# Kernel optimization log

Measured on AMD Instinct MI355X. Metric: run time of the kernel, lower is better.

The kernel has to match this reference:

```python
import jax, jax.numpy as jnp
import numpy as np

MARGIN_SCALE = 0.2
SPATIAL_ALPHA = 0.6
CHANNEL_ALPHA = 0.5
LANG_ALPHA = 0.4
EPS = 1e-06


def _xywh_to_xyxy(boxes):
    xc, yc, w, h = jnp.split(boxes, 4, axis=-1)
    return jnp.concatenate([xc - w / 2.0, yc - h / 2.0, xc + w / 2.0, yc + h / 2.0], axis=-1)


def _clamp_boxes(boxes):
    x1, y1, x2, y2 = [jnp.clip(b[..., 0], 0.0, 1.0) for b in jnp.split(boxes, 4, axis=-1)]
    x_low, x_high = jnp.minimum(x1, x2), jnp.maximum(x1, x2)
    y_low, y_high = jnp.minimum(y1, y2), jnp.maximum(y1, y2)
    w = jnp.maximum(x_high - x_low, EPS)
    h = jnp.maximum(y_high - y_low, EPS)
    cx = (x_high + x_low) * 0.5
    cy = (y_high + y_low) * 0.5
    return jnp.stack([
        jnp.clip(cx - w * 0.5, 0.0, 1.0),
        jnp.clip(cy - h * 0.5, 0.0, 1.0),
        jnp.clip(cx + w * 0.5, 0.0, 1.0),
        jnp.clip(cy + h * 0.5, 0.0, 1.0),
    ], axis=-1)


def _box_to_mask(boxes_xyxy, H, W, margin, dtype):
    # fully vectorized replacement of the per-sample Python loop
    ys = jnp.linspace(0.0, 1.0, H)  # [H]
    xs = jnp.linspace(0.0, 1.0, W)  # [W]
    x1, y1, x2, y2 = [boxes_xyxy[:, i] for i in range(4)]
    mx1 = jnp.clip(x1 - margin, 0.0, 1.0)[:, None, None]
    my1 = jnp.clip(y1 - margin, 0.0, 1.0)[:, None, None]
    mx2 = jnp.clip(x2 + margin, 0.0, 1.0)[:, None, None]
    my2 = jnp.clip(y2 + margin, 0.0, 1.0)[:, None, None]
    xg = xs[None, None, :]  # [1,1,W]
    yg = ys[None, :, None]  # [1,H,1]
    mask = (xg >= mx1) & (xg <= mx2) & (yg >= my1) & (yg <= my2)  # [B,H,W]
    return mask.astype(dtype)[:, None, :, :]  # [B,1,H,W]


def _conv2d(x, w, b, pad):
    out = jax.lax.conv_general_dilated(
        x, w, window_strides=(1, 1), padding=((pad, pad), (pad, pad)),
        dimension_numbers=('NCHW', 'OIHW', 'NCHW'))
    return out + b[None, :, None, None]


def setup_inputs() -> dict:
    key = jax.random.key(0)
    ks = jax.random.split(key, 9)
    B, C, H, W = 32, 256, 64, 64
    s = lambda fan_in: 1.0 / np.sqrt(fan_in)
    return {
        'feat': jax.random.normal(ks[0], (B, C, H, W), jnp.float32),
        'lang_vec': jax.random.normal(ks[1], (B, 256), jnp.float32),
        'pointer_xywh': jax.random.uniform(ks[2], (B, 4), jnp.float32),
        'conv1_w': jax.random.normal(ks[3], (16, 1, 3, 3), jnp.float32) * s(9),
        'conv1_b': jnp.zeros((16,), jnp.float32),
        'conv2_w': jax.random.normal(ks[4], (1, 16, 1, 1), jnp.float32) * s(16),
        'conv2_b': jnp.zeros((1,), jnp.float32),
        'cg_w1': jax.random.normal(ks[5], (256, 512), jnp.float32) * s(512),
        'cg_b1': jnp.zeros((256,), jnp.float32),
        'cg_w2': jax.random.normal(ks[6], (256, 256), jnp.float32) * s(256),
        'cg_b2': jnp.zeros((256,), jnp.float32),
        'lf_w1': jax.random.normal(ks[7], (256, 512), jnp.float32) * s(512),
        'lf_b1': jnp.zeros((256,), jnp.float32),
        'lf_w2': jax.random.normal(ks[8], (256, 256), jnp.float32) * s(256),
        'lf_b2': jnp.zeros((256,), jnp.float32),
    }


def reference(feat, lang_vec, pointer_xywh, conv1_w, conv1_b, conv2_w, conv2_b,
              cg_w1, cg_b1, cg_w2, cg_b2, lf_w1, lf_b1, lf_w2, lf_b2):
    B, C, H, W = feat.shape
    boxes_xyxy = _clamp_boxes(_xywh_to_xyxy(pointer_xywh))
    w = jnp.maximum(boxes_xyxy[:, 2] - boxes_xyxy[:, 0], 1e-4)
    h = jnp.maximum(boxes_xyxy[:, 3] - boxes_xyxy[:, 1], 1e-4)
    diag = jnp.sqrt(w * w + h * h)
    margin = jnp.clip(diag * MARGIN_SCALE, 0.02, 0.2)
    mask = _box_to_mask(boxes_xyxy, H, W, margin, feat.dtype)  # [B,1,H,W]

    # spatial gate: conv3x3 -> relu -> conv1x1 -> sigmoid
    hidden = jax.nn.relu(_conv2d(mask, conv1_w, conv1_b, pad=1))
    refined_mask = jax.nn.sigmoid(_conv2d(hidden, conv2_w, conv2_b, pad=0))  # [B,1,H,W]

    mask_area = jnp.maximum(refined_mask.sum(axis=(2, 3)), 1.0)  # [B,1]
    pointer_feat = (feat * refined_mask).sum(axis=(2, 3)) / mask_area  # [B,C]

    fusion = jnp.concatenate([pointer_feat, lang_vec], axis=1)  # [B, C+256]
    ch_gate = jax.nn.sigmoid(jax.nn.relu(fusion @ cg_w1.T + cg_b1) @ cg_w2.T + cg_b2)
    ch_gate = ch_gate.reshape(B, C, 1, 1)
    lang_delta = jnp.tanh(jax.nn.relu(fusion @ lf_w1.T + lf_b1) @ lf_w2.T + lf_b2)

    guided_feat = feat * (1.0 + SPATIAL_ALPHA * refined_mask) * (1.0 + CHANNEL_ALPHA * ch_gate)
    guided_lang = lang_vec + LANG_ALPHA * lang_delta
    return (guided_feat, guided_lang, boxes_xyxy, refined_mask, pointer_feat)
```

## Files before the change

### kernel.cpp

```cpp
#include <hip/hip_runtime.h>
#include <math.h>

#define B_  32
#define C_  256
#define H_  64
#define W_  64
#define HW  (H_*W_)
#define HW4 (HW/4)

typedef float f32x4 __attribute__((ext_vector_type(4)));

__device__ __forceinline__ float clamp01(float v) {
    return fminf(fmaxf(v, 0.0f), 1.0f);
}

__device__ __forceinline__ float block_reduce_sum_256(float v, float* sm) {
    #pragma unroll
    for (int off = 32; off > 0; off >>= 1) v += __shfl_down(v, off, 64);
    int lane = threadIdx.x & 63, wid = threadIdx.x >> 6;
    if (lane == 0) sm[wid] = v;
    __syncthreads();
    float total = 0.0f;
    if (threadIdx.x == 0) total = sm[0] + sm[1] + sm[2] + sm[3];
    return total;
}

__global__ __launch_bounds__(256) void kern_mask(
    const float* __restrict__ xywh,
    const float* __restrict__ conv1_w, const float* __restrict__ conv1_b,
    const float* __restrict__ conv2_w, const float* __restrict__ conv2_b,
    float* __restrict__ out_boxes, float* __restrict__ out_rm,
    float* __restrict__ ws_part)
{
    const int b = blockIdx.x >> 2;
    const int q = blockIdx.x & 3;
    const int t = threadIdx.x;

    __shared__ float sw1[16 * 9];
    __shared__ float sb1[16];
    __shared__ float sw2[16];
    __shared__ float sred[4];

    if (t < 144)                 sw1[t]       = conv1_w[t];
    else if (t < 160)            sb1[t - 144] = conv1_b[t - 144];
    else if (t < 176)            sw2[t - 160] = conv2_w[t - 160];
    const float b2v = conv2_b[0];

    const float xc = xywh[b * 4 + 0];
    const float yc = xywh[b * 4 + 1];
    const float bw = xywh[b * 4 + 2];
    const float bh = xywh[b * 4 + 3];

    float x1 = clamp01(xc - bw * 0.5f);
    float y1 = clamp01(yc - bh * 0.5f);
    float x2 = clamp01(xc + bw * 0.5f);
    float y2 = clamp01(yc + bh * 0.5f);
    float xl = fminf(x1, x2), xh = fmaxf(x1, x2);
    float yl = fminf(y1, y2), yh = fmaxf(y1, y2);
    float w_ = fmaxf(xh - xl, 1e-6f);
    float h_ = fmaxf(yh - yl, 1e-6f);
    float cx = (xh + xl) * 0.5f, cy = (yh + yl) * 0.5f;
    float bx1 = clamp01(cx - w_ * 0.5f);
    float by1 = clamp01(cy - h_ * 0.5f);
    float bx2 = clamp01(cx + w_ * 0.5f);
    float by2 = clamp01(cy + h_ * 0.5f);

    if (t == 0 && q == 0) {
        out_boxes[b * 4 + 0] = bx1;
        out_boxes[b * 4 + 1] = by1;
        out_boxes[b * 4 + 2] = bx2;
        out_boxes[b * 4 + 3] = by2;
    }

    float ww = fmaxf(bx2 - bx1, 1e-4f);
    float hh = fmaxf(by2 - by1, 1e-4f);
    float diag = sqrtf(ww * ww + hh * hh);
    float margin = fminf(fmaxf(diag * 0.2f, 0.02f), 0.2f);
    float mx1 = clamp01(bx1 - margin);
    float my1 = clamp01(by1 - margin);
    float mx2 = clamp01(bx2 + margin);
    float my2 = clamp01(by2 + margin);

    __syncthreads();

    float asum = 0.0f;
    const int p0 = q * 1024;
    for (int pi = t; pi < 1024; pi += 256) {
        const int p = p0 + pi;
        const int y = p >> 6;
        const int x = p & 63;
        float mv[9];
        #pragma unroll
        for (int ky = 0; ky < 3; ++ky) {
            const int yy = y + ky - 1;
            float gy = (float)((double)yy / 63.0);
            bool yin = (yy >= 0) && (yy < H_) && (gy >= my1) && (gy <= my2);
            #pragma unroll
            for (int kx = 0; kx < 3; ++kx) {
                const int xx = x + kx - 1;
                float gx = (float)((double)xx / 63.0);
                bool xin = (xx >= 0) && (xx < W_) && (gx >= mx1) && (gx <= mx2);
                mv[ky * 3 + kx] = (yin && xin) ? 1.0f : 0.0f;
            }
        }
        float z = b2v;
        #pragma unroll
        for (int oc = 0; oc < 16; ++oc) {
            float hsum = sb1[oc];
            #pragma unroll
            for (int k = 0; k < 9; ++k) hsum = fmaf(mv[k], sw1[oc * 9 + k], hsum);
            z = fmaf(fmaxf(hsum, 0.0f), sw2[oc], z);
        }
        float rm = 1.0f / (1.0f + expf(-z));
        out_rm[b * HW + p] = rm;
        asum += rm;
    }

    float total = block_reduce_sum_256(asum, sred);
    if (t == 0) ws_part[b * 4 + q] = total;
}

__global__ __launch_bounds__(256) void kern_pf(
    const float* __restrict__ feat, const float* __restrict__ rm,
    const float* __restrict__ ws_part, float* __restrict__ out_pf)
{
    const int blk = blockIdx.x;
    const int b = blk >> 7;
    const int c0 = (blk & 127) * 2;
    __shared__ float2 sred[4];

    const size_t row0 = ((size_t)b * C_ + c0) * HW;
    const f32x4* f0 = (const f32x4*)(feat + row0);
    const f32x4* f1 = f0 + HW4;
    const f32x4* r4 = (const f32x4*)(rm + (size_t)b * HW);

    float s0 = 0.0f, s1 = 0.0f;
    for (int i = threadIdx.x; i < HW4; i += 256) {
        f32x4 r = r4[i];
        f32x4 a = f0[i];
        f32x4 c = f1[i];
        s0 = fmaf(a.x, r.x, fmaf(a.y, r.y, fmaf(a.z, r.z, fmaf(a.w, r.w, s0))));
        s1 = fmaf(c.x, r.x, fmaf(c.y, r.y, fmaf(c.z, r.z, fmaf(c.w, r.w, s1))));
    }
    #pragma unroll
    for (int off = 32; off > 0; off >>= 1) {
        s0 += __shfl_down(s0, off, 64);
        s1 += __shfl_down(s1, off, 64);
    }
    int lane = threadIdx.x & 63, wid = threadIdx.x >> 6;
    if (lane == 0) sred[wid] = make_float2(s0, s1);
    __syncthreads();
    if (threadIdx.x == 0) {
        float t0 = sred[0].x + sred[1].x + sred[2].x + sred[3].x;
        float t1 = sred[0].y + sred[1].y + sred[2].y + sred[3].y;
        float area = fmaxf(ws_part[b * 4 + 0] + ws_part[b * 4 + 1] +
                           ws_part[b * 4 + 2] + ws_part[b * 4 + 3], 1.0f);
        out_pf[b * C_ + c0]     = t0 / area;
        out_pf[b * C_ + c0 + 1] = t1 / area;
    }
}

__global__ __launch_bounds__(256) void kern_mlp(
    const float* __restrict__ pf, const float* __restrict__ lang,
    const float* __restrict__ cg_w1, const float* __restrict__ cg_b1,
    const float* __restrict__ cg_w2, const float* __restrict__ cg_b2,
    const float* __restrict__ lf_w1, const float* __restrict__ lf_b1,
    const float* __restrict__ lf_w2, const float* __restrict__ lf_b2,
    float* __restrict__ ws_cg, float* __restrict__ out_gl)
{
    const int b = blockIdx.x >> 1;
    const int which = blockIdx.x & 1;
    const int t = threadIdx.x;
    __shared__ float fus[512];
    __shared__ float hid[256];

    fus[t]       = pf[b * 256 + t];
    fus[256 + t] = lang[b * 256 + t];

    const float* w1 = which ? lf_w1 : cg_w1;
    const float* b1 = which ? lf_b1 : cg_b1;
    const float* w2 = which ? lf_w2 : cg_w2;
    const float* b2 = which ? lf_b2 : cg_b2;
    __syncthreads();

    const f32x4* wv = (const f32x4*)(w1 + (size_t)t * 512);
    const f32x4* fv = (const f32x4*)fus;
    float s = 0.0f;
    #pragma unroll 4
    for (int k = 0; k < 128; ++k) {
        f32x4 f = fv[k], w = wv[k];
        s = fmaf(f.x, w.x, fmaf(f.y, w.y, fmaf(f.z, w.z, fmaf(f.w, w.w, s))));
    }
    hid[t] = fmaxf(s + b1[t], 0.0f);
    __syncthreads();

    const f32x4* w2v = (const f32x4*)(w2 + (size_t)t * 256);
    const f32x4* hv = (const f32x4*)hid;
    float s2 = 0.0f;
    #pragma unroll 4
    for (int k = 0; k < 64; ++k) {
        f32x4 h = hv[k], w = w2v[k];
        s2 = fmaf(h.x, w.x, fmaf(h.y, w.y, fmaf(h.z, w.z, fmaf(h.w, w.w, s2))));
    }
    s2 += b2[t];
    if (which == 0) {
        ws_cg[b * 256 + t] = 1.0f / (1.0f + expf(-s2));
    } else {
        out_gl[b * 256 + t] = fus[256 + t] + 0.4f * tanhf(s2);
    }
}

__global__ __launch_bounds__(256) void kern_guided(
    const float* __restrict__ feat, const float* __restrict__ rm,
    const float* __restrict__ ws_cg, float* __restrict__ out_gf)
{
    const int blk = blockIdx.x;
    const int b = blk >> 7;
    const int c0 = (blk & 127) * 2;
    const float g0 = 1.0f + 0.5f * ws_cg[b * C_ + c0];
    const float g1 = 1.0f + 0.5f * ws_cg[b * C_ + c0 + 1];

    const size_t row0 = ((size_t)b * C_ + c0) * HW;
    const f32x4* f0 = (const f32x4*)(feat + row0);
    const f32x4* f1 = f0 + HW4;
    const f32x4* r4 = (const f32x4*)(rm + (size_t)b * HW);
    f32x4* o0 = (f32x4*)(out_gf + row0);
    f32x4* o1 = o0 + HW4;

    for (int i = threadIdx.x; i < HW4; i += 256) {
        f32x4 r = r4[i];
        f32x4 m;
        m.x = 1.0f + 0.6f * r.x;
        m.y = 1.0f + 0.6f * r.y;
        m.z = 1.0f + 0.6f * r.z;
        m.w = 1.0f + 0.6f * r.w;
        f32x4 a = f0[i];
        f32x4 c = f1[i];
        f32x4 oa, ob;
        oa.x = a.x * m.x * g0;  oa.y = a.y * m.y * g0;
        oa.z = a.z * m.z * g0;  oa.w = a.w * m.w * g0;
        ob.x = c.x * m.x * g1;  ob.y = c.y * m.y * g1;
        ob.z = c.z * m.z * g1;  ob.w = c.w * m.w * g1;
        __builtin_nontemporal_store(oa, &o0[i]);
        __builtin_nontemporal_store(ob, &o1[i]);
    }
}

extern "C" void kernel_launch(void* const* d_in, const int* in_sizes, int n_in,
                              void* d_out, int out_size, void* d_ws, size_t ws_size,
                              hipStream_t stream) {
    const float* feat     = (const float*)d_in[0];
    const float* lang     = (const float*)d_in[1];
    const float* xywh     = (const float*)d_in[2];
    const float* conv1_w  = (const float*)d_in[3];
    const float* conv1_b  = (const float*)d_in[4];
    const float* conv2_w  = (const float*)d_in[5];
    const float* conv2_b  = (const float*)d_in[6];
    const float* cg_w1    = (const float*)d_in[7];
    const float* cg_b1    = (const float*)d_in[8];
    const float* cg_w2    = (const float*)d_in[9];
    const float* cg_b2    = (const float*)d_in[10];
    const float* lf_w1    = (const float*)d_in[11];
    const float* lf_b1    = (const float*)d_in[12];
    const float* lf_w2    = (const float*)d_in[13];
    const float* lf_b2    = (const float*)d_in[14];

    float* out = (float*)d_out;
    const size_t N_GF = (size_t)B_ * C_ * HW;
    float* out_gf    = out;
    float* out_gl    = out_gf + N_GF;
    float* out_boxes = out_gl + (size_t)B_ * C_;
    float* out_rm    = out_boxes + B_ * 4;
    float* out_pf    = out_rm + (size_t)B_ * HW;

    float* wsf     = (float*)d_ws;
    float* ws_part = wsf;
    float* ws_cg   = wsf + 128;
    float* ws_pf   = ws_cg + B_ * C_;

    (void)ws_pf; (void)ws_size; (void)in_sizes; (void)n_in; (void)out_size;

    kern_mask<<<B_ * 4, 256, 0, stream>>>(xywh, conv1_w, conv1_b, conv2_w, conv2_b,
                                          out_boxes, out_rm, ws_part);
    kern_pf<<<B_ * C_ / 2, 256, 0, stream>>>(feat, out_rm, ws_part, out_pf);
    kern_mlp<<<B_ * 2, 256, 0, stream>>>(out_pf, lang,
                                         cg_w1, cg_b1, cg_w2, cg_b2,
                                         lf_w1, lf_b1, lf_w2, lf_b2,
                                         ws_cg, out_gl);
    kern_guided<<<B_ * C_ / 2, 256, 0, stream>>>(feat, out_rm, ws_cg, out_gf);
}
```

Baseline: 95.14 us.

## Fuse pointer-feature reduction with spatial-gate write, then rescale output in place

```diff
diff --git a/kernel.cpp b/kernel.cpp
--- a/kernel.cpp
+++ b/kernel.cpp
@@ -7,22 +7,12 @@
 #define W_  64
 #define HW  (H_*W_)
 #define HW4 (HW/4)
+#define RPB 4
 
 typedef float f32x4 __attribute__((ext_vector_type(4)));
 
 __device__ __forceinline__ float clamp01(float v) {
     return fminf(fmaxf(v, 0.0f), 1.0f);
-}
-
-__device__ __forceinline__ float block_reduce_sum_256(float v, float* sm) {
-    #pragma unroll
-    for (int off = 32; off > 0; off >>= 1) v += __shfl_down(v, off, 64);
-    int lane = threadIdx.x & 63, wid = threadIdx.x >> 6;
-    if (lane == 0) sm[wid] = v;
-    __syncthreads();
-    float total = 0.0f;
-    if (threadIdx.x == 0) total = sm[0] + sm[1] + sm[2] + sm[3];
-    return total;
 }
 
 __global__ __launch_bounds__(256) void kern_mask(
@@ -116,47 +106,78 @@
         asum += rm;
     }
 
-    float total = block_reduce_sum_256(asum, sred);
-    if (t == 0) ws_part[b * 4 + q] = total;
-}
-
-__global__ __launch_bounds__(256) void kern_pf(
+    #pragma unroll
+    for (int off = 32; off > 0; off >>= 1) asum += __shfl_down(asum, off, 64);
+    int lane = t & 63, wid = t >> 6;
+    if (lane == 0) sred[wid] = asum;
+    __syncthreads();
+    if (t == 0) ws_part[b * 4 + q] = sred[0] + sred[1] + sred[2] + sred[3];
+}
+
+__global__ __launch_bounds__(256) void kern_pf_fused(
     const float* __restrict__ feat, const float* __restrict__ rm,
-    const float* __restrict__ ws_part, float* __restrict__ out_pf)
+    const float* __restrict__ ws_part, float* __restrict__ out_pf,
+    float* __restrict__ out_gf)
 {
     const int blk = blockIdx.x;
-    const int b = blk >> 7;
-    const int c0 = (blk & 127) * 2;
-    __shared__ float2 sred[4];
+    const int b = blk >> 6;
+    const int c0 = (blk & 63) * RPB;
+    __shared__ f32x4 sred[4];
 
     const size_t row0 = ((size_t)b * C_ + c0) * HW;
-    const f32x4* f0 = (const f32x4*)(feat + row0);
-    const f32x4* f1 = f0 + HW4;
+    const f32x4* fr = (const f32x4*)(feat + row0);
+    f32x4* orow = (f32x4*)(out_gf + row0);
     const f32x4* r4 = (const f32x4*)(rm + (size_t)b * HW);
 
-    float s0 = 0.0f, s1 = 0.0f;
+    float s0 = 0.f, s1 = 0.f, s2 = 0.f, s3 = 0.f;
     for (int i = threadIdx.x; i < HW4; i += 256) {
         f32x4 r = r4[i];
-        f32x4 a = f0[i];
-        f32x4 c = f1[i];
-        s0 = fmaf(a.x, r.x, fmaf(a.y, r.y, fmaf(a.z, r.z, fmaf(a.w, r.w, s0))));
-        s1 = fmaf(c.x, r.x, fmaf(c.y, r.y, fmaf(c.z, r.z, fmaf(c.w, r.w, s1))));
-    }
+        f32x4 m;
+        m.x = 1.0f + 0.6f * r.x;
+        m.y = 1.0f + 0.6f * r.y;
+        m.z = 1.0f + 0.6f * r.z;
+        m.w = 1.0f + 0.6f * r.w;
+
+        f32x4 f0 = __builtin_nontemporal_load(&fr[i]);
+        f32x4 f1 = __builtin_nontemporal_load(&fr[i + HW4]);
+        f32x4 f2 = __builtin_nontemporal_load(&fr[i + 2 * HW4]);
+        f32x4 f3 = __builtin_nontemporal_load(&fr[i + 3 * HW4]);
+
+        s0 = fmaf(f0.x, r.x, fmaf(f0.y, r.y, fmaf(f0.z, r.z, fmaf(f0.w, r.w, s0))));
+        s1 = fmaf(f1.x, r.x, fmaf(f1.y, r.y, fmaf(f1.z, r.z, fmaf(f1.w, r.w, s1))));
+        s2 = fmaf(f2.x, r.x, fmaf(f2.y, r.y, fmaf(f2.z, r.z, fmaf(f2.w, r.w, s2))));
+        s3 = fmaf(f3.x, r.x, fmaf(f3.y, r.y, fmaf(f3.z, r.z, fmaf(f3.w, r.w, s3))));
+
+        f32x4 o0, o1, o2, o3;
+        o0.x = f0.x * m.x; o0.y = f0.y * m.y; o0.z = f0.z * m.z; o0.w = f0.w * m.w;
+        o1.x = f1.x * m.x; o1.y = f1.y * m.y; o1.z = f1.z * m.z; o1.w = f1.w * m.w;
+        o2.x = f2.x * m.x; o2.y = f2.y * m.y; o2.z = f2.z * m.z; o2.w = f2.w * m.w;
+        o3.x = f3.x * m.x; o3.y = f3.y * m.y; o3.z = f3.z * m.z; o3.w = f3.w * m.w;
+        orow[i]           = o0;
+        orow[i + HW4]     = o1;
+        orow[i + 2*HW4]   = o2;
+        orow[i + 3*HW4]   = o3;
+    }
+
     #pragma unroll
     for (int off = 32; off > 0; off >>= 1) {
         s0 += __shfl_down(s0, off, 64);
         s1 += __shfl_down(s1, off, 64);
+        s2 += __shfl_down(s2, off, 64);
+        s3 += __shfl_down(s3, off, 64);
     }
     int lane = threadIdx.x & 63, wid = threadIdx.x >> 6;
-    if (lane == 0) sred[wid] = make_float2(s0, s1);
+    if (lane == 0) { f32x4 v; v.x = s0; v.y = s1; v.z = s2; v.w = s3; sred[wid] = v; }
     __syncthreads();
     if (threadIdx.x == 0) {
-        float t0 = sred[0].x + sred[1].x + sred[2].x + sred[3].x;
-        float t1 = sred[0].y + sred[1].y + sred[2].y + sred[3].y;
         float area = fmaxf(ws_part[b * 4 + 0] + ws_part[b * 4 + 1] +
                            ws_part[b * 4 + 2] + ws_part[b * 4 + 3], 1.0f);
-        out_pf[b * C_ + c0]     = t0 / area;
-        out_pf[b * C_ + c0 + 1] = t1 / area;
+        float inv = 1.0f / area;
+        f32x4 t0 = sred[0], t1 = sred[1], t2 = sred[2], t3 = sred[3];
+        out_pf[b * C_ + c0 + 0] = (t0.x + t1.x + t2.x + t3.x) * inv;
+        out_pf[b * C_ + c0 + 1] = (t0.y + t1.y + t2.y + t3.y) * inv;
+        out_pf[b * C_ + c0 + 2] = (t0.z + t1.z + t2.z + t3.z) * inv;
+        out_pf[b * C_ + c0 + 3] = (t0.w + t1.w + t2.w + t3.w) * inv;
     }
 }
 
@@ -210,39 +231,32 @@
     }
 }
 
-__global__ __launch_bounds__(256) void kern_guided(
-    const float* __restrict__ feat, const float* __restrict__ rm,
+__global__ __launch_bounds__(256) void kern_scale(
     const float* __restrict__ ws_cg, float* __restrict__ out_gf)
 {
     const int blk = blockIdx.x;
-    const int b = blk >> 7;
-    const int c0 = (blk & 127) * 2;
-    const float g0 = 1.0f + 0.5f * ws_cg[b * C_ + c0];
+    const int b = blk >> 6;
+    const int c0 = (blk & 63) * RPB;
+    const float g0 = 1.0f + 0.5f * ws_cg[b * C_ + c0 + 0];
     const float g1 = 1.0f + 0.5f * ws_cg[b * C_ + c0 + 1];
-
-    const size_t row0 = ((size_t)b * C_ + c0) * HW;
-    const f32x4* f0 = (const f32x4*)(feat + row0);
-    const f32x4* f1 = f0 + HW4;
-    const f32x4* r4 = (const f32x4*)(rm + (size_t)b * HW);
-    f32x4* o0 = (f32x4*)(out_gf + row0);
-    f32x4* o1 = o0 + HW4;
+    const float g2 = 1.0f + 0.5f * ws_cg[b * C_ + c0 + 2];
+    const float g3 = 1.0f + 0.5f * ws_cg[b * C_ + c0 + 3];
+
+    f32x4* o = (f32x4*)(out_gf + ((size_t)b * C_ + c0) * HW);
 
     for (int i = threadIdx.x; i < HW4; i += 256) {
-        f32x4 r = r4[i];
-        f32x4 m;
-        m.x = 1.0f + 0.6f * r.x;
-        m.y = 1.0f + 0.6f * r.y;
-        m.z = 1.0f + 0.6f * r.z;
-        m.w = 1.0f + 0.6f * r.w;
-        f32x4 a = f0[i];
-        f32x4 c = f1[i];
-        f32x4 oa, ob;
-        oa.x = a.x * m.x * g0;  oa.y = a.y * m.y * g0;
-        oa.z = a.z * m.z * g0;  oa.w = a.w * m.w * g0;
-        ob.x = c.x * m.x * g1;  ob.y = c.y * m.y * g1;
-        ob.z = c.z * m.z * g1;  ob.w = c.w * m.w * g1;
-        __builtin_nontemporal_store(oa, &o0[i]);
-        __builtin_nontemporal_store(ob, &o1[i]);
+        f32x4 a = o[i];
+        f32x4 b1v = o[i + HW4];
+        f32x4 c = o[i + 2 * HW4];
+        f32x4 d = o[i + 3 * HW4];
+        a.x *= g0; a.y *= g0; a.z *= g0; a.w *= g0;
+        b1v.x *= g1; b1v.y *= g1; b1v.z *= g1; b1v.w *= g1;
+        c.x *= g2; c.y *= g2; c.z *= g2; c.w *= g2;
+        d.x *= g3; d.y *= g3; d.z *= g3; d.w *= g3;
+        o[i]           = a;
+        o[i + HW4]     = b1v;
+        o[i + 2*HW4]   = c;
+        o[i + 3*HW4]   = d;
     }
 }
 
@@ -276,16 +290,16 @@
     float* wsf     = (float*)d_ws;
     float* ws_part = wsf;
     float* ws_cg   = wsf + 128;
-    float* ws_pf   = ws_cg + B_ * C_;
-
-    (void)ws_pf; (void)ws_size; (void)in_sizes; (void)n_in; (void)out_size;
+
+    (void)ws_size; (void)in_sizes; (void)n_in; (void)out_size;
 
     kern_mask<<<B_ * 4, 256, 0, stream>>>(xywh, conv1_w, conv1_b, conv2_w, conv2_b,
                                           out_boxes, out_rm, ws_part);
-    kern_pf<<<B_ * C_ / 2, 256, 0, stream>>>(feat, out_rm, ws_part, out_pf);
+    kern_pf_fused<<<B_ * C_ / RPB, 256, 0, stream>>>(feat, out_rm, ws_part,
+                                                     out_pf, out_gf);
     kern_mlp<<<B_ * 2, 256, 0, stream>>>(out_pf, lang,
                                          cg_w1, cg_b1, cg_w2, cg_b2,
                                          lf_w1, lf_b1, lf_w2, lf_b2,
                                          ws_cg, out_gl);
-    kern_guided<<<B_ * C_ / 2, 256, 0, stream>>>(feat, out_rm, ws_cg, out_gf);
-}
+    kern_scale<<<B_ * C_ / RPB, 256, 0, stream>>>(ws_cg, out_gf);
+}
```

Measured after the change: 116.5 us. 1.22x slower.

## Fuse channel-gate MLP into guided-feature kernel and widen rows per block

Applied to the files above, without the earlier changes.

```diff
diff --git a/kernel.cpp b/kernel.cpp
--- a/kernel.cpp
+++ b/kernel.cpp
@@ -7,22 +7,13 @@
 #define W_  64
 #define HW  (H_*W_)
 #define HW4 (HW/4)
+#define PF_RPB 8
+#define GD_RPB 16
 
 typedef float f32x4 __attribute__((ext_vector_type(4)));
 
 __device__ __forceinline__ float clamp01(float v) {
     return fminf(fmaxf(v, 0.0f), 1.0f);
-}
-
-__device__ __forceinline__ float block_reduce_sum_256(float v, float* sm) {
-    #pragma unroll
-    for (int off = 32; off > 0; off >>= 1) v += __shfl_down(v, off, 64);
-    int lane = threadIdx.x & 63, wid = threadIdx.x >> 6;
-    if (lane == 0) sm[wid] = v;
-    __syncthreads();
-    float total = 0.0f;
-    if (threadIdx.x == 0) total = sm[0] + sm[1] + sm[2] + sm[3];
-    return total;
 }
 
 __global__ __launch_bounds__(256) void kern_mask(
@@ -116,8 +107,12 @@
         asum += rm;
     }
 
-    float total = block_reduce_sum_256(asum, sred);
-    if (t == 0) ws_part[b * 4 + q] = total;
+    #pragma unroll
+    for (int off = 32; off > 0; off >>= 1) asum += __shfl_down(asum, off, 64);
+    int lane = t & 63, wid = t >> 6;
+    if (lane == 0) sred[wid] = asum;
+    __syncthreads();
+    if (t == 0) ws_part[b * 4 + q] = sred[0] + sred[1] + sred[2] + sred[3];
 }
 
 __global__ __launch_bounds__(256) void kern_pf(
@@ -125,124 +120,148 @@
     const float* __restrict__ ws_part, float* __restrict__ out_pf)
 {
     const int blk = blockIdx.x;
-    const int b = blk >> 7;
-    const int c0 = (blk & 127) * 2;
-    __shared__ float2 sred[4];
+    const int b = blk >> 5;
+    const int c0 = (blk & 31) * PF_RPB;
+    __shared__ float sred[4][PF_RPB];
 
     const size_t row0 = ((size_t)b * C_ + c0) * HW;
-    const f32x4* f0 = (const f32x4*)(feat + row0);
-    const f32x4* f1 = f0 + HW4;
+    const f32x4* fr = (const f32x4*)(feat + row0);
     const f32x4* r4 = (const f32x4*)(rm + (size_t)b * HW);
 
-    float s0 = 0.0f, s1 = 0.0f;
+    float s[PF_RPB];
+    #pragma unroll
+    for (int j = 0; j < PF_RPB; ++j) s[j] = 0.0f;
+
     for (int i = threadIdx.x; i < HW4; i += 256) {
         f32x4 r = r4[i];
-        f32x4 a = f0[i];
-        f32x4 c = f1[i];
-        s0 = fmaf(a.x, r.x, fmaf(a.y, r.y, fmaf(a.z, r.z, fmaf(a.w, r.w, s0))));
-        s1 = fmaf(c.x, r.x, fmaf(c.y, r.y, fmaf(c.z, r.z, fmaf(c.w, r.w, s1))));
-    }
+        #pragma unroll
+        for (int j = 0; j < PF_RPB; ++j) {
+            f32x4 f = fr[i + j * HW4];
+            s[j] = fmaf(f.x, r.x, fmaf(f.y, r.y, fmaf(f.z, r.z, fmaf(f.w, r.w, s[j]))));
+        }
+    }
+
     #pragma unroll
-    for (int off = 32; off > 0; off >>= 1) {
-        s0 += __shfl_down(s0, off, 64);
-        s1 += __shfl_down(s1, off, 64);
+    for (int j = 0; j < PF_RPB; ++j) {
+        #pragma unroll
+        for (int off = 32; off > 0; off >>= 1) s[j] += __shfl_down(s[j], off, 64);
     }
     int lane = threadIdx.x & 63, wid = threadIdx.x >> 6;
-    if (lane == 0) sred[wid] = make_float2(s0, s1);
-    __syncthreads();
-    if (threadIdx.x == 0) {
-        float t0 = sred[0].x + sred[1].x + sred[2].x + sred[3].x;
-        float t1 = sred[0].y + sred[1].y + sred[2].y + sred[3].y;
+    if (lane == 0) {
+        #pragma unroll
+        for (int j = 0; j < PF_RPB; ++j) sred[wid][j] = s[j];
+    }
+    __syncthreads();
+    if (threadIdx.x < PF_RPB) {
+        int j = threadIdx.x;
         float area = fmaxf(ws_part[b * 4 + 0] + ws_part[b * 4 + 1] +
                            ws_part[b * 4 + 2] + ws_part[b * 4 + 3], 1.0f);
-        out_pf[b * C_ + c0]     = t0 / area;
-        out_pf[b * C_ + c0 + 1] = t1 / area;
-    }
-}
-
-__global__ __launch_bounds__(256) void kern_mlp(
+        float tot = sred[0][j] + sred[1][j] + sred[2][j] + sred[3][j];
+        out_pf[b * C_ + c0 + j] = tot / area;
+    }
+}
+
+__global__ __launch_bounds__(256) void kern_guided(
+    const float* __restrict__ feat, const float* __restrict__ rm,
     const float* __restrict__ pf, const float* __restrict__ lang,
     const float* __restrict__ cg_w1, const float* __restrict__ cg_b1,
     const float* __restrict__ cg_w2, const float* __restrict__ cg_b2,
     const float* __restrict__ lf_w1, const float* __restrict__ lf_b1,
     const float* __restrict__ lf_w2, const float* __restrict__ lf_b2,
-    float* __restrict__ ws_cg, float* __restrict__ out_gl)
+    float* __restrict__ out_gl, float* __restrict__ out_gf)
 {
-    const int b = blockIdx.x >> 1;
-    const int which = blockIdx.x & 1;
+    const int blk = blockIdx.x;
+    const int b = blk >> 4;
+    const int g = blk & 15;
+    const int c0 = g * GD_RPB;
     const int t = threadIdx.x;
+
     __shared__ float fus[512];
     __shared__ float hid[256];
+    __shared__ float hid_lf[256];
+    __shared__ float gates[GD_RPB];
 
     fus[t]       = pf[b * 256 + t];
     fus[256 + t] = lang[b * 256 + t];
-
-    const float* w1 = which ? lf_w1 : cg_w1;
-    const float* b1 = which ? lf_b1 : cg_b1;
-    const float* w2 = which ? lf_w2 : cg_w2;
-    const float* b2 = which ? lf_b2 : cg_b2;
-    __syncthreads();
-
-    const f32x4* wv = (const f32x4*)(w1 + (size_t)t * 512);
-    const f32x4* fv = (const f32x4*)fus;
-    float s = 0.0f;
-    #pragma unroll 4
-    for (int k = 0; k < 128; ++k) {
-        f32x4 f = fv[k], w = wv[k];
-        s = fmaf(f.x, w.x, fmaf(f.y, w.y, fmaf(f.z, w.z, fmaf(f.w, w.w, s))));
-    }
-    hid[t] = fmaxf(s + b1[t], 0.0f);
-    __syncthreads();
-
-    const f32x4* w2v = (const f32x4*)(w2 + (size_t)t * 256);
-    const f32x4* hv = (const f32x4*)hid;
-    float s2 = 0.0f;
-    #pragma unroll 4
-    for (int k = 0; k < 64; ++k) {
-        f32x4 h = hv[k], w = w2v[k];
-        s2 = fmaf(h.x, w.x, fmaf(h.y, w.y, fmaf(h.z, w.z, fmaf(h.w, w.w, s2))));
-    }
-    s2 += b2[t];
-    if (which == 0) {
-        ws_cg[b * 256 + t] = 1.0f / (1.0f + expf(-s2));
-    } else {
-        out_gl[b * 256 + t] = fus[256 + t] + 0.4f * tanhf(s2);
-    }
-}
-
-__global__ __launch_bounds__(256) void kern_guided(
-    const float* __restrict__ feat, const float* __restrict__ rm,
-    const float* __restrict__ ws_cg, float* __restrict__ out_gf)
-{
-    const int blk = blockIdx.x;
-    const int b = blk >> 7;
-    const int c0 = (blk & 127) * 2;
-    const float g0 = 1.0f + 0.5f * ws_cg[b * C_ + c0];
-    const float g1 = 1.0f + 0.5f * ws_cg[b * C_ + c0 + 1];
+    __syncthreads();
+
+    {
+        const f32x4* wv = (const f32x4*)(cg_w1 + (size_t)t * 512);
+        const f32x4* fv = (const f32x4*)fus;
+        float s = 0.0f;
+        #pragma unroll 8
+        for (int k = 0; k < 128; ++k) {
+            f32x4 f = fv[k], w = wv[k];
+            s = fmaf(f.x, w.x, fmaf(f.y, w.y, fmaf(f.z, w.z, fmaf(f.w, w.w, s))));
+        }
+        hid[t] = fmaxf(s + cg_b1[t], 0.0f);
+    }
+    __syncthreads();
+
+    if (t < GD_RPB) {
+        const int c = c0 + t;
+        const f32x4* wv = (const f32x4*)(cg_w2 + (size_t)c * 256);
+        const f32x4* hv = (const f32x4*)hid;
+        float s = 0.0f;
+        #pragma unroll 8
+        for (int k = 0; k < 64; ++k) {
+            f32x4 h = hv[k], w = wv[k];
+            s = fmaf(h.x, w.x, fmaf(h.y, w.y, fmaf(h.z, w.z, fmaf(h.w, w.w, s))));
+        }
+        s += cg_b2[c];
+        gates[t] = 1.0f + 0.5f / (1.0f + expf(-s));
+    }
+    if (g == 0) {
+        const f32x4* wv = (const f32x4*)(lf_w1 + (size_t)t * 512);
+        const f32x4* fv = (const f32x4*)fus;
+        float s = 0.0f;
+        #pragma unroll 8
+        for (int k = 0; k < 128; ++k) {
+            f32x4 f = fv[k], w = wv[k];
+            s = fmaf(f.x, w.x, fmaf(f.y, w.y, fmaf(f.z, w.z, fmaf(f.w, w.w, s))));
+        }
+        hid_lf[t] = fmaxf(s + lf_b1[t], 0.0f);
+    }
+    __syncthreads();
+
+    if (g == 0) {
+        const f32x4* wv = (const f32x4*)(lf_w2 + (size_t)t * 256);
+        const f32x4* hv = (const f32x4*)hid_lf;
+        float s = 0.0f;
+        #pragma unroll 8
+        for (int k = 0; k < 64; ++k) {
+            f32x4 h = hv[k], w = wv[k];
+            s = fmaf(h.x, w.x, fmaf(h.y, w.y, fmaf(h.z, w.z, fmaf(h.w, w.w, s))));
+        }
+        out_gl[b * 256 + t] = fus[256 + t] + 0.4f * tanhf(s + lf_b2[t]);
+    }
+
+    float gr[GD_RPB];
+    #pragma unroll
+    for (int j = 0; j < GD_RPB; ++j) gr[j] = gates[j];
 
     const size_t row0 = ((size_t)b * C_ + c0) * HW;
-    const f32x4* f0 = (const f32x4*)(feat + row0);
-    const f32x4* f1 = f0 + HW4;
+    const f32x4* fr = (const f32x4*)(feat + row0);
+    f32x4* orow = (f32x4*)(out_gf + row0);
     const f32x4* r4 = (const f32x4*)(rm + (size_t)b * HW);
-    f32x4* o0 = (f32x4*)(out_gf + row0);
-    f32x4* o1 = o0 + HW4;
-
-    for (int i = threadIdx.x; i < HW4; i += 256) {
+
+    for (int i = t; i < HW4; i += 256) {
         f32x4 r = r4[i];
         f32x4 m;
         m.x = 1.0f + 0.6f * r.x;
         m.y = 1.0f + 0.6f * r.y;
         m.z = 1.0f + 0.6f * r.z;
         m.w = 1.0f + 0.6f * r.w;
-        f32x4 a = f0[i];
-        f32x4 c = f1[i];
-        f32x4 oa, ob;
-        oa.x = a.x * m.x * g0;  oa.y = a.y * m.y * g0;
-        oa.z = a.z * m.z * g0;  oa.w = a.w * m.w * g0;
-        ob.x = c.x * m.x * g1;  ob.y = c.y * m.y * g1;
-        ob.z = c.z * m.z * g1;  ob.w = c.w * m.w * g1;
-        __builtin_nontemporal_store(oa, &o0[i]);
-        __builtin_nontemporal_store(ob, &o1[i]);
+        #pragma unroll
+        for (int j = 0; j < GD_RPB; ++j) {
+            f32x4 f = fr[i + j * HW4];
+            f32x4 o;
+            o.x = f.x * m.x * gr[j];
+            o.y = f.y * m.y * gr[j];
+            o.z = f.z * m.z * gr[j];
+            o.w = f.w * m.w * gr[j];
+            __builtin_nontemporal_store(o, &orow[i + j * HW4]);
+        }
     }
 }
 
@@ -275,17 +294,14 @@
 
     float* wsf     = (float*)d_ws;
     float* ws_part = wsf;
-    float* ws_cg   = wsf + 128;
-    float* ws_pf   = ws_cg + B_ * C_;
-
-    (void)ws_pf; (void)ws_size; (void)in_sizes; (void)n_in; (void)out_size;
+
+    (void)ws_size; (void)in_sizes; (void)n_in; (void)out_size;
 
     kern_mask<<<B_ * 4, 256, 0, stream>>>(xywh, conv1_w, conv1_b, conv2_w, conv2_b,
                                           out_boxes, out_rm, ws_part);
-    kern_pf<<<B_ * C_ / 2, 256, 0, stream>>>(feat, out_rm, ws_part, out_pf);
-    kern_mlp<<<B_ * 2, 256, 0, stream>>>(out_pf, lang,
-                                         cg_w1, cg_b1, cg_w2, cg_b2,
-                                         lf_w1, lf_b1, lf_w2, lf_b2,
-                                         ws_cg, out_gl);
-    kern_guided<<<B_ * C_ / 2, 256, 0, stream>>>(feat, out_rm, ws_cg, out_gf);
-}
+    kern_pf<<<B_ * C_ / PF_RPB, 256, 0, stream>>>(feat, out_rm, ws_part, out_pf);
+    kern_guided<<<B_ * C_ / GD_RPB, 256, 0, stream>>>(feat, out_rm, out_pf, lang,
+                                                      cg_w1, cg_b1, cg_w2, cg_b2,
+                                                      lf_w1, lf_b1, lf_w2, lf_b2,
+                                                      out_gl, out_gf);
+}
```

Measured after the change: 123.6 us. 1.3x slower.
